# Kernel optimization log

Hardware: AMD Instinct MI355X
Metric: run time of the kernel (lower is better)

## Reference

```python
import jax, jax.numpy as jnp
import numpy as np

B, T, D = 2, 2048, 1024   # batch, seq, d_model
E, K, H = 8, 2, 704       # routed experts, topk, expert hidden
SH = 704 * 2              # shared-expert hidden = moe_hidden * num_shared_experts
EPS = 1e-20               # topk_norm_epsilon
STD = 0.02                # init_weight_std


def setup_inputs() -> dict:
    key = jax.random.key(0)
    ks = jax.random.split(key, 8)
    return {
        "x":   jax.random.normal(ks[0], (B, T, D), jnp.float32),
        "Wg":  jax.random.normal(ks[1], (E, D), jnp.float32) * STD,   # router experts_weights
        "W1":  jax.random.normal(ks[2], (E, D, H), jnp.float32) * STD,  # gate proj per expert
        "W3":  jax.random.normal(ks[3], (E, D, H), jnp.float32) * STD,  # up proj per expert
        "W2":  jax.random.normal(ks[4], (E, H, D), jnp.float32) * STD,  # down proj per expert
        "Ws1": jax.random.normal(ks[5], (D, SH), jnp.float32) * STD,    # shared expert
        "Ws3": jax.random.normal(ks[6], (D, SH), jnp.float32) * STD,
        "Ws2": jax.random.normal(ks[7], (SH, D), jnp.float32) * STD,
    }


def reference(x, Wg, W1, W3, W2, Ws1, Ws3, Ws2):
    b, t, d = x.shape
    n = b * t
    xf = x.reshape(n, d)
    # softmax gating + topk + scatter back into dense [N,E] gate matrix
    gates = jax.nn.softmax(xf @ Wg.T, axis=-1)                      # [N,E]
    top_v, top_i = jax.lax.top_k(gates, K)                          # [N,K]
    masked = jnp.zeros_like(gates).at[jnp.arange(n)[:, None], top_i].set(top_v)
    masked = masked / (masked.sum(-1, keepdims=True) + EPS)         # normalized_moe_gates
    # per-expert SwiGLU FFN over all tokens, then gate-weighted combine
    h = jnp.einsum('nd,edh->enh', xf, W1)                           # [E,N,H]
    g = jnp.einsum('nd,edh->enh', xf, W3)
    y = jnp.einsum('enh,ehd->end', jax.nn.silu(h) * g, W2)          # [E,N,D]
    routed = jnp.einsum('ne,end->nd', masked, y)                    # combine
    shared = (jax.nn.silu(xf @ Ws1) * (xf @ Ws3)) @ Ws2             # shared experts
    return (routed + shared).reshape(b, t, d)
```

## Files before the change

### kernel.cpp

```cpp
#include <hip/hip_runtime.h>
#include <math.h>

typedef __bf16 bf16;
typedef __attribute__((ext_vector_type(8))) __bf16 bf16x8;
typedef __attribute__((ext_vector_type(4))) __bf16 bf16x4;
typedef __attribute__((ext_vector_type(4))) float f32x4;

#define NTOK 4096
#define DM   1024
#define NE   8
#define NEX  10
#define HE   704

#define MAP1_CAP 224
#define MAP2_CAP 160

#define OFF_CNT   0u
#define OFF_TOK   256u
#define OFF_WGT   131328u
#define OFF_XB    262400u
#define OFF_W1T   8651008u
#define OFF_W3T   20185344u
#define OFF_W2T   31719680u
#define OFF_WS1T  43254016u
#define OFF_WS3T  46137600u
#define OFF_WS2T  49021184u
#define OFF_ACT   51904768u
#define OFF_EIDS  74973440u
#define OFF_MAP1  OFF_EIDS
#define OFF_MAP2  (OFF_EIDS + 8192u)
#define OFF_GW    74989824u
#define OFF_SLOT  75022592u
#define OFF_YR    OFF_W1T

__device__ __forceinline__ void async_cp16(const bf16* g, bf16* l)
{
    __builtin_amdgcn_global_load_lds(
        (const __attribute__((address_space(1))) unsigned int*)g,
        (__attribute__((address_space(3))) unsigned int*)l, 16, 0, 0);
}

__global__ __launch_bounds__(256) void prep_all(
    const float* __restrict__ x,  const float* __restrict__ Wg,
    const float* __restrict__ W1, const float* __restrict__ W3, const float* __restrict__ W2,
    const float* __restrict__ Ws1, const float* __restrict__ Ws3, const float* __restrict__ Ws2,
    bf16* __restrict__ w1t, bf16* __restrict__ w3t, bf16* __restrict__ w2t,
    bf16* __restrict__ ws1t, bf16* __restrict__ ws3t, bf16* __restrict__ ws2t,
    bf16* __restrict__ xb, int* __restrict__ eids, float2* __restrict__ gw)
{
    int id = blockIdx.x;
    if (id < 21120) {
        const float* src; bf16* dst; int C, rt, ct, nkt;
        if (id < 5632)       { int t = id;         int e = t / 704, m = t % 704; C = 704;
                               src = W1 + (size_t)e * 1024 * 704;  dst = w1t + (size_t)e * 720896;
                               ct = m % 22; rt = m / 22; nkt = 32; }
        else if (id < 11264) { int t = id - 5632;  int e = t / 704, m = t % 704; C = 704;
                               src = W3 + (size_t)e * 1024 * 704;  dst = w3t + (size_t)e * 720896;
                               ct = m % 22; rt = m / 22; nkt = 32; }
        else if (id < 16896) { int t = id - 11264; int e = t / 704, m = t % 704; C = 1024;
                               src = W2 + (size_t)e * 704 * 1024;  dst = w2t + (size_t)e * 720896;
                               ct = m % 32; rt = m / 32; nkt = 22; }
        else if (id < 18304) { int t = id - 16896; C = 1408; src = Ws1;
                               ct = t % 44; rt = t / 44; nkt = 32;
                               int ep = (ct >= 22) ? 1 : 0; ct -= 22 * ep;
                               src += (size_t)704 * ep;
                               dst = ws1t + (size_t)ep * 720896; }
        else if (id < 19712) { int t = id - 18304; C = 1408; src = Ws3;
                               ct = t % 44; rt = t / 44; nkt = 32;
                               int ep = (ct >= 22) ? 1 : 0; ct -= 22 * ep;
                               src += (size_t)704 * ep;
                               dst = ws3t + (size_t)ep * 720896; }
        else                 { int t = id - 19712; C = 1024; src = Ws2;
                               ct = t % 32; rt = t / 32; nkt = 22;
                               int ep = (rt >= 22) ? 1 : 0; rt -= 22 * ep;
                               src += (size_t)704 * 1024 * ep;
                               dst = ws2t + (size_t)ep * 720896; }

        __shared__ float tl[32][33];
        int c0 = ct * 32, r0 = rt * 32;
        int row  = threadIdx.x >> 3;
        int col4 = (threadIdx.x & 7) * 4;
        float4 v = *(const float4*)&src[(size_t)(r0 + row) * C + c0 + col4];
        tl[row][col4 + 0] = v.x; tl[row][col4 + 1] = v.y;
        tl[row][col4 + 2] = v.z; tl[row][col4 + 3] = v.w;
        __syncthreads();
        int t2   = threadIdx.x;
        int half = t2 >> 7;
        int ei   = (t2 & 127) * 4;
        int cc   = ei >> 7;
        int nr   = (ei >> 3) & 15;
        int jj   = ei & 7;
        int n_loc = half * 16 + nr;
        int k_loc = cc * 8 + jj;
        bf16x4 o;
        o[0] = (bf16)tl[k_loc + 0][n_loc];
        o[1] = (bf16)tl[k_loc + 1][n_loc];
        o[2] = (bf16)tl[k_loc + 2][n_loc];
        o[3] = (bf16)tl[k_loc + 3][n_loc];
        int ng = ct * 2 + half;
        *(bf16x4*)&dst[(size_t)(((ng * nkt + rt) << 9) + ei)] = o;
        return;
    }
    id -= 21120;
    if (id < 4096) {
        int i = id * 256 + threadIdx.x;
        float4 v = ((const float4*)x)[i];
        bf16x4 o;
        o[0] = (bf16)v.x; o[1] = (bf16)v.y; o[2] = (bf16)v.z; o[3] = (bf16)v.w;
        ((bf16x4*)xb)[i] = o;
        return;
    }
    id -= 4096;
    {
        int n    = id * 4 + (threadIdx.x >> 6);
        int lane = threadIdx.x & 63;
        const float* xrow = x + (size_t)n * DM;
        float xr[16];
        #pragma unroll
        for (int j = 0; j < 16; j++) xr[j] = xrow[lane + 64 * j];
        float logit[NE];
        #pragma unroll
        for (int e = 0; e < NE; e++) {
            const float* wr = Wg + e * DM;
            float s = 0.f;
            #pragma unroll
            for (int j = 0; j < 16; j++) s += xr[j] * wr[lane + 64 * j];
            #pragma unroll
            for (int off = 32; off; off >>= 1) s += __shfl_xor(s, off, 64);
            logit[e] = s;
        }
        if (lane == 0) {
            int i0 = 0;
            #pragma unroll
            for (int e = 1; e < NE; e++) if (logit[e] > logit[i0]) i0 = e;
            int i1 = (i0 == 0) ? 1 : 0;
            #pragma unroll
            for (int e = 0; e < NE; e++) if (e != i0 && logit[e] > logit[i1]) i1 = e;
            float m = logit[0];
            #pragma unroll
            for (int e = 1; e < NE; e++) m = fmaxf(m, logit[e]);
            float denom = 0.f;
            #pragma unroll
            for (int e = 0; e < NE; e++) denom += expf(logit[e] - m);
            float g0 = expf(logit[i0] - m) / denom;
            float g1 = expf(logit[i1] - m) / denom;
            float inv = 1.f / (g0 + g1 + 1e-20f);
            eids[n] = i0 | (i1 << 16);
            gw[n] = make_float2(g0 * inv, g1 * inv);
        }
    }
}

__global__ __launch_bounds__(128) void build_lists(
    const int* __restrict__ eids, const float2* __restrict__ gw,
    int* __restrict__ cnt, int* __restrict__ tok, float* __restrict__ wgt,
    int2* __restrict__ slots)
{
    __shared__ int lcnt[NE];
    __shared__ int gbase[NE];
    int t = threadIdx.x;
    int n = blockIdx.x * 128 + t;
    if (t < NE) lcnt[t] = 0;
    __syncthreads();
    int packed = eids[n];
    float2 w = gw[n];
    int e0 = packed & 0xffff, e1 = packed >> 16;
    int s0 = atomicAdd(&lcnt[e0], 1);
    int s1 = atomicAdd(&lcnt[e1], 1);
    __syncthreads();
    if (t < NE) gbase[t] = atomicAdd(&cnt[t], lcnt[t]);
    __syncthreads();
    int p0 = gbase[e0] + s0, p1 = gbase[e1] + s1;
    tok[e0 * NTOK + p0] = n; wgt[e0 * NTOK + p0] = w.x;
    tok[e1 * NTOK + p1] = n; wgt[e1 * NTOK + p1] = w.y;
    slots[n] = make_int2((e0 << 16) | p0, (e1 << 16) | p1);
}

__global__ void prefix_kernel(const int* __restrict__ cnt, int* __restrict__ pfx,
                              int* __restrict__ map1, int* __restrict__ map2)
{
    __shared__ int sx1[144], ss1[144], se1[144];
    __shared__ int sx2[112], ss2[112], se2[112];
    __shared__ int ns1s, ns2s;
    int t = threadIdx.x;
    for (int i = t; i < 8 * MAP1_CAP; i += 64) map1[i] = -1;
    for (int i = t; i < 8 * MAP2_CAP; i += 64) map2[i] = -1;

    if (t == 0) {
        int s = 0;
        for (int e = 0; e < NEX; e++) { pfx[e] = s; s += (e < NE) ? cnt[e] : NTOK; }
        pfx[NEX] = s;

        int ntl[NEX];
        int tot1 = 0;
        for (int e = 0; e < NEX; e++) {
            int c = (e < NE) ? cnt[e] : NTOK;
            ntl[e] = (c + 127) >> 7;
            tot1 += ntl[e];
        }
        {
            int len[8] = {0,0,0,0,0,0,0,0};
            int avg = (tot1 * 11 + 7) >> 3;
            int ns = 0, k = 0;
            for (int e = 0; e < NEX; e++) {
                k = 0;
                for (int q = 1; q < 8; q++) if (len[q] < len[k]) k = q;
                for (int tt = 0; tt < ntl[e]; tt++) {
                    if (len[k] >= avg) {
                        k = 0;
                        for (int q = 1; q < 8; q++) if (len[q] < len[k]) k = q;
                    }
                    if (len[k] + 11 > MAP1_CAP) {
                        k = 0;
                        for (int q = 1; q < 8; q++) if (len[q] < len[k]) k = q;
                    }
                    sx1[ns] = k; ss1[ns] = len[k]; se1[ns] = (e << 20) | (tt << 8);
                    len[k] += 11; ns++;
                }
            }
            ns1s = ns;
        }
        {
            int wrk[8] = {0,0,0,0,0,0,0,0};
            int slt[8] = {0,0,0,0,0,0,0,0};
            int totw = 0;
            for (int e = 0; e <= NE; e++)
                totw += (e < NE) ? ntl[e] * 8 * 22 : (NTOK >> 7) * 8 * 44;
            int avg = (totw + 7) >> 3;
            int ns = 0, k = 0;
            for (int e = 0; e <= NE; e++) {
                int nt2 = (e < NE) ? ntl[e] : (NTOK >> 7);
                int wpd = (e < NE) ? 22 : 44;
                k = 0;
                for (int q = 1; q < 8; q++) if (wrk[q] < wrk[k]) k = q;
                for (int tt = 0; tt < nt2; tt++) {
                    if (wrk[k] >= avg) {
                        k = 0;
                        for (int q = 1; q < 8; q++) if (wrk[q] < wrk[k]) k = q;
                    }
                    if (slt[k] + 8 > MAP2_CAP) {
                        k = 0;
                        for (int q = 1; q < 8; q++) if (slt[q] < slt[k]) k = q;
                    }
                    sx2[ns] = k; ss2[ns] = slt[k]; se2[ns] = (e << 20) | (tt << 8);
                    slt[k] += 8; wrk[k] += 8 * wpd; ns++;
                }
            }
            ns2s = ns;
        }
    }
    __syncthreads();
    int n1 = ns1s, n2 = ns2s;
    for (int i = t; i < n1 * 11; i += 64) {
        int sg = i / 11, h = i - sg * 11;
        map1[(ss1[sg] + h) * 8 + sx1[sg]] = se1[sg] | h;
    }
    for (int i = t; i < n2 * 8; i += 64) {
        int sg = i >> 3, d = i & 7;
        map2[(ss2[sg] + d) * 8 + sx2[sg]] = se2[sg] | d;
    }
}

__global__ __launch_bounds__(256) void gemm1_swiglu(
    const bf16* __restrict__ xb,
    const bf16* __restrict__ w1t, const bf16* __restrict__ w3t,
    const bf16* __restrict__ ws1t, const bf16* __restrict__ ws3t,
    bf16* __restrict__ act,
    const int* __restrict__ cnt, const int* __restrict__ pfx,
    const int* __restrict__ tok, const int* __restrict__ map)
{
    int b = blockIdx.x;
    int ent = map[(b >> 3) * 8 + (b & 7)];
    if (ent < 0) return;
    int e  = ent >> 20;
    int m0 = ((ent >> 8) & 0xfff) << 7;
    int h0 = (ent & 255) * 64;
    int count = (e < NE) ? cnt[e] : NTOK;
    int base = pfx[e];
    const bf16 *B1, *B3;
    if (e < NE) { B1 = w1t + (size_t)e * 720896;         B3 = w3t + (size_t)e * 720896; }
    else        { B1 = ws1t + (size_t)(e - NE) * 720896; B3 = ws3t + (size_t)(e - NE) * 720896; }
    const int* tlist = (e < NE) ? tok + e * NTOK : nullptr;

    __shared__ bf16 As[3][8 * 512];
    __shared__ bf16 B1s[3][4 * 512];
    __shared__ bf16 B3s[3][4 * 512];

    int tid = threadIdx.x, w = tid >> 6, lane = tid & 63;

    int r3 = lane >> 2;
    int cx = (lane & 3) ^ ((r3 >> 1) & 3);
    int sA0 = m0 + 32 * w + r3, sA1 = sA0 + 16;
    int rA0 = tlist ? (sA0 < count ? tlist[sA0] : 0) : (sA0 < count ? sA0 : 0);
    int rA1 = tlist ? (sA1 < count ? tlist[sA1] : 0) : (sA1 < count ? sA1 : 0);
    const bf16* ga0 = xb + (size_t)rA0 * DM + cx * 8;
    const bf16* ga1 = xb + (size_t)rA1 * DM + cx * 8;
    const bf16* gb1 = B1 + ((size_t)((h0 >> 4) + w) * 32) * 512 + lane * 8;
    const bf16* gb3 = B3 + ((size_t)((h0 >> 4) + w) * 32) * 512 + lane * 8;
    bf16* aA0 = &As[0][0]  + (2 * w) * 512;
    bf16* aA1 = aA0 + 512;
    bf16* aB1 = &B1s[0][0] + w * 512;
    bf16* aB3 = &B3s[0][0] + w * 512;

    int rl = lane & 15, ch = lane >> 4;
    int uA = 4 * rl + (ch ^ ((rl >> 1) & 3));
    int gA = (w & 1) * 4;
    int gB = (w >> 1) * 2;
    int wm = (w & 1) * 64, wn = (w >> 1) * 32;

    f32x4 acch[4][2], accg[4][2];
    #pragma unroll
    for (int i = 0; i < 4; i++)
        #pragma unroll
        for (int j = 0; j < 2; j++) {
            acch[i][j] = (f32x4){0.f, 0.f, 0.f, 0.f};
            accg[i][j] = (f32x4){0.f, 0.f, 0.f, 0.f};
        }

#define STAGE1(bs) do { \
        async_cp16(ga0, aA0 + (bs) * 4096); \
        async_cp16(ga1, aA1 + (bs) * 4096); \
        async_cp16(gb1, aB1 + (bs) * 2048); \
        async_cp16(gb3, aB3 + (bs) * 2048); \
        ga0 += 32; ga1 += 32; gb1 += 512; gb3 += 512; \
    } while (0)

    STAGE1(0);
    STAGE1(1);
    asm volatile("s_waitcnt vmcnt(4)" ::: "memory");
    __builtin_amdgcn_s_barrier();

    int rb = 0, sb = 2;
    for (int k0 = 0; k0 < 32; k0++) {
        const bf16* Ab  = &As[0][0]  + rb * 4096;
        const bf16* B1b = &B1s[0][0] + rb * 2048;
        const bf16* B3b = &B3s[0][0] + rb * 2048;
        bf16x8 af[4], b1f[2], b3f[2];
        #pragma unroll
        for (int i = 0; i < 4; i++) af[i] = *(const bf16x8*)(Ab + (gA + i) * 512 + uA * 8);
        #pragma unroll
        for (int j = 0; j < 2; j++) {
            b1f[j] = *(const bf16x8*)(B1b + (gB + j) * 512 + lane * 8);
            b3f[j] = *(const bf16x8*)(B3b + (gB + j) * 512 + lane * 8);
        }
        if (k0 < 30) STAGE1(sb);
        #pragma unroll
        for (int i = 0; i < 4; i++)
            #pragma unroll
            for (int j = 0; j < 2; j++) {
                acch[i][j] = __builtin_amdgcn_mfma_f32_16x16x32_bf16(af[i], b1f[j], acch[i][j], 0, 0, 0);
                accg[i][j] = __builtin_amdgcn_mfma_f32_16x16x32_bf16(af[i], b3f[j], accg[i][j], 0, 0, 0);
            }
        if (k0 < 30)       asm volatile("s_waitcnt vmcnt(4)" ::: "memory");
        else if (k0 == 30) asm volatile("s_waitcnt vmcnt(0)" ::: "memory");
        __builtin_amdgcn_sched_barrier(0);
        __builtin_amdgcn_s_barrier();
        rb = (rb == 2) ? 0 : rb + 1;
        sb = (sb == 2) ? 0 : sb + 1;
    }
#undef STAGE1

    #pragma unroll
    for (int i = 0; i < 4; i++)
        #pragma unroll
        for (int j = 0; j < 2; j++)
            #pragma unroll
            for (int r = 0; r < 4; r++) {
                int row = wm + i * 16 + ch * 4 + r;
                int s2 = m0 + row;
                if (s2 < count) {
                    float hv = acch[i][j][r], gv = accg[i][j][r];
                    float a = hv / (1.f + expf(-hv)) * gv;
                    act[(size_t)(base + s2) * HE + h0 + wn + j * 16 + rl] = (bf16)a;
                }
            }
}

__global__ __launch_bounds__(256) void gemm2_all(
    const bf16* __restrict__ act,
    const bf16* __restrict__ w2t, const bf16* __restrict__ ws2t,
    bf16* __restrict__ yr, float* __restrict__ out,
    const int* __restrict__ cnt, const int* __restrict__ pfx,
    const float* __restrict__ wgt, const int* __restrict__ map)
{
    int b = blockIdx.x;
    int ent = map[(b >> 3) * 8 + (b & 7)];
    if (ent < 0) return;
    int e  = ent >> 20;
    int m0 = ((ent >> 8) & 0xfff) << 7;
    int d0 = (ent & 255) * 128;

    __shared__ bf16 As[3][8 * 512];
    __shared__ bf16 Bs[3][8 * 512];

    int tid = threadIdx.x, w = tid >> 6, lane = tid & 63;

    int r3 = lane >> 2;
    int cx = (lane & 3) ^ ((r3 >> 1) & 3);
    int sA0 = m0 + 32 * w + r3, sA1 = sA0 + 16;
    int rl = lane & 15, ch = lane >> 4;
    int uA = 4 * rl + (ch ^ ((rl >> 1) & 3));
    int gA = (w & 1) * 4, gB = (w >> 1) * 4;
    int wm = (w & 1) * 64, wn = (w >> 1) * 64;

    bf16* aA0 = &As[0][0] + (2 * w) * 512;
    bf16* aA1 = aA0 + 512;
    bf16* aB0 = &Bs[0][0] + (2 * w) * 512;
    bf16* aB1 = aB0 + 512;

    int count, base; const bf16* Bp;
    if (e < NE) { count = cnt[e]; base = pfx[e]; Bp = w2t + (size_t)e * 720896; }
    else        { count = NTOK;   base = NTOK * 2; Bp = ws2t; }

    int a0 = (sA0 < count) ? (base + sA0) : base;
    int a1 = (sA1 < count) ? (base + sA1) : base;
    const bf16* ga0 = act + (size_t)a0 * HE + cx * 8;
    const bf16* ga1 = act + (size_t)a1 * HE + cx * 8;
    const bf16* gb0 = Bp + ((size_t)((d0 >> 4) + 2 * w) * 22) * 512 + lane * 8;
    const bf16* gb1 = Bp + ((size_t)((d0 >> 4) + 2 * w + 1) * 22) * 512 + lane * 8;

    f32x4 acc[4][4];
    #pragma unroll
    for (int i = 0; i < 4; i++)
        #pragma unroll
        for (int j = 0; j < 4; j++) acc[i][j] = (f32x4){0.f, 0.f, 0.f, 0.f};

#define STAGE2(bs) do { \
        async_cp16(ga0, aA0 + (bs) * 4096); \
        async_cp16(ga1, aA1 + (bs) * 4096); \
        async_cp16(gb0, aB0 + (bs) * 4096); \
        async_cp16(gb1, aB1 + (bs) * 4096); \
        ga0 += 32; ga1 += 32; gb0 += 512; gb1 += 512; \
    } while (0)

    int total = (e < NE) ? 22 : 44;
    STAGE2(0);
    STAGE2(1);
    asm volatile("s_waitcnt vmcnt(4)" ::: "memory");
    __builtin_amdgcn_s_barrier();

    int rb = 0, sb = 2;
    for (int kt = 0; kt < total; kt++) {
        const bf16* Ab = &As[0][0] + rb * 4096;
        const bf16* Bb = &Bs[0][0] + rb * 4096;
        bf16x8 af[4], bf_[4];
        #pragma unroll
        for (int i = 0; i < 4; i++) af[i]  = *(const bf16x8*)(Ab + (gA + i) * 512 + uA * 8);
        #pragma unroll
        for (int j = 0; j < 4; j++) bf_[j] = *(const bf16x8*)(Bb + (gB + j) * 512 + lane * 8);
        int nx = kt + 2;
        if (nx < total) {
            if (nx == 22) {
                ga0 = act + (size_t)(12288 + sA0) * HE + cx * 8;
                ga1 = act + (size_t)(12288 + sA1) * HE + cx * 8;
                const bf16* B2 = ws2t + 720896;
                gb0 = B2 + ((size_t)((d0 >> 4) + 2 * w) * 22) * 512 + lane * 8;
                gb1 = B2 + ((size_t)((d0 >> 4) + 2 * w + 1) * 22) * 512 + lane * 8;
            }
            STAGE2(sb);
        }
        #pragma unroll
        for (int i = 0; i < 4; i++)
            #pragma unroll
            for (int j = 0; j < 4; j++)
                acc[i][j] = __builtin_amdgcn_mfma_f32_16x16x32_bf16(af[i], bf_[j], acc[i][j], 0, 0, 0);
        if (nx < total)       asm volatile("s_waitcnt vmcnt(4)" ::: "memory");
        else if (nx == total) asm volatile("s_waitcnt vmcnt(0)" ::: "memory");
        __builtin_amdgcn_sched_barrier(0);
        __builtin_amdgcn_s_barrier();
        rb = (rb == 2) ? 0 : rb + 1;
        sb = (sb == 2) ? 0 : sb + 1;
    }
#undef STAGE2

    if (e < NE) {
        const float* wl = wgt + e * NTOK;
        #pragma unroll
        for (int i = 0; i < 4; i++) {
            #pragma unroll
            for (int r = 0; r < 4; r++) {
                int row = wm + i * 16 + ch * 4 + r;
                int s2 = m0 + row;
                if (s2 < count) {
                    float wt = wl[s2];
                    bf16* yrow = yr + (size_t)(base + s2) * DM + d0 + wn;
                    #pragma unroll
                    for (int j = 0; j < 4; j++)
                        yrow[j * 16 + rl] = (bf16)(wt * acc[i][j][r]);
                }
            }
        }
    } else {
        #pragma unroll
        for (int i = 0; i < 4; i++) {
            #pragma unroll
            for (int r = 0; r < 4; r++) {
                int row = wm + i * 16 + ch * 4 + r;
                float* orow = out + (size_t)(m0 + row) * DM + d0 + wn;
                #pragma unroll
                for (int j = 0; j < 4; j++)
                    orow[j * 16 + rl] = acc[i][j][r];
            }
        }
    }
}

__global__ __launch_bounds__(256) void fuse_add(
    const bf16* __restrict__ yr, const int2* __restrict__ slots,
    const int* __restrict__ pfx, float* __restrict__ out)
{
    int n = blockIdx.x;
    int2 s = slots[n];
    int slot0 = pfx[s.x >> 16] + (s.x & 0xffff);
    int slot1 = pfx[s.y >> 16] + (s.y & 0xffff);
    const bf16* y0 = yr + (size_t)slot0 * DM;
    const bf16* y1 = yr + (size_t)slot1 * DM;
    float* orow = out + (size_t)n * DM;
    int d = threadIdx.x * 4;
    bf16x4 a = *(const bf16x4*)(y0 + d);
    bf16x4 b = *(const bf16x4*)(y1 + d);
    float4 o = *(float4*)(orow + d);
    o.x += (float)a[0] + (float)b[0];
    o.y += (float)a[1] + (float)b[1];
    o.z += (float)a[2] + (float)b[2];
    o.w += (float)a[3] + (float)b[3];
    *(float4*)(orow + d) = o;
}

extern "C" void kernel_launch(void* const* d_in, const int* in_sizes, int n_in,
                              void* d_out, int out_size, void* d_ws, size_t ws_size,
                              hipStream_t stream)
{
    const float* x   = (const float*)d_in[0];
    const float* Wg  = (const float*)d_in[1];
    const float* W1  = (const float*)d_in[2];
    const float* W3  = (const float*)d_in[3];
    const float* W2  = (const float*)d_in[4];
    const float* Ws1 = (const float*)d_in[5];
    const float* Ws3 = (const float*)d_in[6];
    const float* Ws2 = (const float*)d_in[7];
    float* out = (float*)d_out;
    char*  ws  = (char*)d_ws;

    int*    cnt   = (int*)(ws + OFF_CNT);
    int*    pfx   = (int*)(ws + OFF_CNT + 32);
    int*    tok   = (int*)(ws + OFF_TOK);
    float*  wgt   = (float*)(ws + OFF_WGT);
    bf16*   xb    = (bf16*)(ws + OFF_XB);
    bf16*   w1t   = (bf16*)(ws + OFF_W1T);
    bf16*   w3t   = (bf16*)(ws + OFF_W3T);
    bf16*   w2t   = (bf16*)(ws + OFF_W2T);
    bf16*   ws1t  = (bf16*)(ws + OFF_WS1T);
    bf16*   ws3t  = (bf16*)(ws + OFF_WS3T);
    bf16*   ws2t  = (bf16*)(ws + OFF_WS2T);
    bf16*   act   = (bf16*)(ws + OFF_ACT);
    int*    eids  = (int*)(ws + OFF_EIDS);
    int*    map1  = (int*)(ws + OFF_MAP1);
    int*    map2  = (int*)(ws + OFF_MAP2);
    float2* gw    = (float2*)(ws + OFF_GW);
    int2*   slots = (int2*)(ws + OFF_SLOT);
    bf16*   yr    = (bf16*)(ws + OFF_YR);

    hipMemsetAsync(ws, 0, 256, stream);

    prep_all<<<21120 + 4096 + 1024, 256, 0, stream>>>(
        x, Wg, W1, W3, W2, Ws1, Ws3, Ws2,
        w1t, w3t, w2t, ws1t, ws3t, ws2t, xb, eids, gw);

    build_lists<<<32, 128, 0, stream>>>(eids, gw, cnt, tok, wgt, slots);
    prefix_kernel<<<1, 64, 0, stream>>>(cnt, pfx, map1, map2);

    gemm1_swiglu<<<8 * MAP1_CAP, 256, 0, stream>>>(
        xb, w1t, w3t, ws1t, ws3t, act, cnt, pfx, tok, map1);

    gemm2_all<<<8 * MAP2_CAP, 256, 0, stream>>>(
        act, w2t, ws2t, yr, out, cnt, pfx, wgt, map2);

    fuse_add<<<NTOK, 256, 0, stream>>>(yr, slots, pfx, out);
}
```

Measured before the change: 308.6 us.

## Fuse routing kernels into one block and deepen GEMM pipelines to four stages

Replaces the memset, the list-building kernel and the prefix kernel with a single 1024-thread block that counts, scatters and builds the schedule maps in one launch using shared-memory atomics only. Both grouped GEMM kernels move from triple to quadruple LDS buffering, with three stages prefetched and adjusted waitcnt thresholds. This removes two launches and hides more global-load latency. The cost is more LDS per block, which may reduce occupancy, and a serial single-block routing step.

After: 309.0 us. About the same (+0.1%).

```diff
diff --git a/kernel.cpp b/kernel.cpp
--- a/kernel.cpp
+++ b/kernel.cpp
@@ -151,50 +151,44 @@
     }
 }
 
-__global__ __launch_bounds__(128) void build_lists(
+__global__ __launch_bounds__(1024) void route_all(
     const int* __restrict__ eids, const float2* __restrict__ gw,
-    int* __restrict__ cnt, int* __restrict__ tok, float* __restrict__ wgt,
-    int2* __restrict__ slots)
+    int* __restrict__ cnt, int* __restrict__ pfx,
+    int* __restrict__ tok, float* __restrict__ wgt, int2* __restrict__ slots,
+    int* __restrict__ map1, int* __restrict__ map2)
 {
     __shared__ int lcnt[NE];
-    __shared__ int gbase[NE];
-    int t = threadIdx.x;
-    int n = blockIdx.x * 128 + t;
-    if (t < NE) lcnt[t] = 0;
-    __syncthreads();
-    int packed = eids[n];
-    float2 w = gw[n];
-    int e0 = packed & 0xffff, e1 = packed >> 16;
-    int s0 = atomicAdd(&lcnt[e0], 1);
-    int s1 = atomicAdd(&lcnt[e1], 1);
-    __syncthreads();
-    if (t < NE) gbase[t] = atomicAdd(&cnt[t], lcnt[t]);
-    __syncthreads();
-    int p0 = gbase[e0] + s0, p1 = gbase[e1] + s1;
-    tok[e0 * NTOK + p0] = n; wgt[e0 * NTOK + p0] = w.x;
-    tok[e1 * NTOK + p1] = n; wgt[e1 * NTOK + p1] = w.y;
-    slots[n] = make_int2((e0 << 16) | p0, (e1 << 16) | p1);
-}
-
-__global__ void prefix_kernel(const int* __restrict__ cnt, int* __restrict__ pfx,
-                              int* __restrict__ map1, int* __restrict__ map2)
-{
     __shared__ int sx1[144], ss1[144], se1[144];
     __shared__ int sx2[112], ss2[112], se2[112];
     __shared__ int ns1s, ns2s;
     int t = threadIdx.x;
-    for (int i = t; i < 8 * MAP1_CAP; i += 64) map1[i] = -1;
-    for (int i = t; i < 8 * MAP2_CAP; i += 64) map2[i] = -1;
-
+    if (t < NE) lcnt[t] = 0;
+    __syncthreads();
+    #pragma unroll
+    for (int c = 0; c < 4; c++) {
+        int n = c * 1024 + t;
+        int packed = eids[n];
+        float2 w = gw[n];
+        int e0 = packed & 0xffff, e1 = packed >> 16;
+        int p0 = atomicAdd(&lcnt[e0], 1);
+        int p1 = atomicAdd(&lcnt[e1], 1);
+        tok[e0 * NTOK + p0] = n; wgt[e0 * NTOK + p0] = w.x;
+        tok[e1 * NTOK + p1] = n; wgt[e1 * NTOK + p1] = w.y;
+        slots[n] = make_int2((e0 << 16) | p0, (e1 << 16) | p1);
+    }
+    __syncthreads();
+    if (t < NE) cnt[t] = lcnt[t];
+    for (int i = t; i < 8 * MAP1_CAP; i += 1024) map1[i] = -1;
+    for (int i = t; i < 8 * MAP2_CAP; i += 1024) map2[i] = -1;
     if (t == 0) {
         int s = 0;
-        for (int e = 0; e < NEX; e++) { pfx[e] = s; s += (e < NE) ? cnt[e] : NTOK; }
+        for (int e = 0; e < NEX; e++) { pfx[e] = s; s += (e < NE) ? lcnt[e] : NTOK; }
         pfx[NEX] = s;
 
         int ntl[NEX];
         int tot1 = 0;
         for (int e = 0; e < NEX; e++) {
-            int c = (e < NE) ? cnt[e] : NTOK;
+            int c = (e < NE) ? lcnt[e] : NTOK;
             ntl[e] = (c + 127) >> 7;
             tot1 += ntl[e];
         }
@@ -251,11 +245,11 @@
     }
     __syncthreads();
     int n1 = ns1s, n2 = ns2s;
-    for (int i = t; i < n1 * 11; i += 64) {
+    for (int i = t; i < n1 * 11; i += 1024) {
         int sg = i / 11, h = i - sg * 11;
         map1[(ss1[sg] + h) * 8 + sx1[sg]] = se1[sg] | h;
     }
-    for (int i = t; i < n2 * 8; i += 64) {
+    for (int i = t; i < n2 * 8; i += 1024) {
         int sg = i >> 3, d = i & 7;
         map2[(ss2[sg] + d) * 8 + sx2[sg]] = se2[sg] | d;
     }
@@ -282,9 +276,9 @@
     else        { B1 = ws1t + (size_t)(e - NE) * 720896; B3 = ws3t + (size_t)(e - NE) * 720896; }
     const int* tlist = (e < NE) ? tok + e * NTOK : nullptr;
 
-    __shared__ bf16 As[3][8 * 512];
-    __shared__ bf16 B1s[3][4 * 512];
-    __shared__ bf16 B3s[3][4 * 512];
+    __shared__ bf16 As[4][8 * 512];
+    __shared__ bf16 B1s[4][4 * 512];
+    __shared__ bf16 B3s[4][4 * 512];
 
     int tid = threadIdx.x, w = tid >> 6, lane = tid & 63;
 
@@ -325,12 +319,11 @@
         ga0 += 32; ga1 += 32; gb1 += 512; gb3 += 512; \
     } while (0)
 
-    STAGE1(0);
-    STAGE1(1);
-    asm volatile("s_waitcnt vmcnt(4)" ::: "memory");
+    STAGE1(0); STAGE1(1); STAGE1(2);
+    asm volatile("s_waitcnt vmcnt(8)" ::: "memory");
     __builtin_amdgcn_s_barrier();
 
-    int rb = 0, sb = 2;
+    int rb = 0, sb = 3;
     for (int k0 = 0; k0 < 32; k0++) {
         const bf16* Ab  = &As[0][0]  + rb * 4096;
         const bf16* B1b = &B1s[0][0] + rb * 2048;
@@ -343,7 +336,7 @@
             b1f[j] = *(const bf16x8*)(B1b + (gB + j) * 512 + lane * 8);
             b3f[j] = *(const bf16x8*)(B3b + (gB + j) * 512 + lane * 8);
         }
-        if (k0 < 30) STAGE1(sb);
+        if (k0 <= 28) STAGE1(sb);
         #pragma unroll
         for (int i = 0; i < 4; i++)
             #pragma unroll
@@ -351,12 +344,13 @@
                 acch[i][j] = __builtin_amdgcn_mfma_f32_16x16x32_bf16(af[i], b1f[j], acch[i][j], 0, 0, 0);
                 accg[i][j] = __builtin_amdgcn_mfma_f32_16x16x32_bf16(af[i], b3f[j], accg[i][j], 0, 0, 0);
             }
-        if (k0 < 30)       asm volatile("s_waitcnt vmcnt(4)" ::: "memory");
+        if (k0 <= 28)      asm volatile("s_waitcnt vmcnt(8)" ::: "memory");
+        else if (k0 == 29) asm volatile("s_waitcnt vmcnt(4)" ::: "memory");
         else if (k0 == 30) asm volatile("s_waitcnt vmcnt(0)" ::: "memory");
         __builtin_amdgcn_sched_barrier(0);
         __builtin_amdgcn_s_barrier();
-        rb = (rb == 2) ? 0 : rb + 1;
-        sb = (sb == 2) ? 0 : sb + 1;
+        rb = (rb + 1) & 3;
+        sb = (sb + 1) & 3;
     }
 #undef STAGE1
 
@@ -390,8 +384,8 @@
     int m0 = ((ent >> 8) & 0xfff) << 7;
     int d0 = (ent & 255) * 128;
 
-    __shared__ bf16 As[3][8 * 512];
-    __shared__ bf16 Bs[3][8 * 512];
+    __shared__ bf16 As[4][8 * 512];
+    __shared__ bf16 Bs[4][8 * 512];
 
     int tid = threadIdx.x, w = tid >> 6, lane = tid & 63;
 
@@ -434,12 +428,11 @@
     } while (0)
 
     int total = (e < NE) ? 22 : 44;
-    STAGE2(0);
-    STAGE2(1);
-    asm volatile("s_waitcnt vmcnt(4)" ::: "memory");
+    STAGE2(0); STAGE2(1); STAGE2(2);
+    asm volatile("s_waitcnt vmcnt(8)" ::: "memory");
     __builtin_amdgcn_s_barrier();
 
-    int rb = 0, sb = 2;
+    int rb = 0, sb = 3;
     for (int kt = 0; kt < total; kt++) {
         const bf16* Ab = &As[0][0] + rb * 4096;
         const bf16* Bb = &Bs[0][0] + rb * 4096;
@@ -448,7 +441,7 @@
         for (int i = 0; i < 4; i++) af[i]  = *(const bf16x8*)(Ab + (gA + i) * 512 + uA * 8);
         #pragma unroll
         for (int j = 0; j < 4; j++) bf_[j] = *(const bf16x8*)(Bb + (gB + j) * 512 + lane * 8);
-        int nx = kt + 2;
+        int nx = kt + 3;
         if (nx < total) {
             if (nx == 22) {
                 ga0 = act + (size_t)(12288 + sA0) * HE + cx * 8;
@@ -464,12 +457,13 @@
             #pragma unroll
             for (int j = 0; j < 4; j++)
                 acc[i][j] = __builtin_amdgcn_mfma_f32_16x16x32_bf16(af[i], bf_[j], acc[i][j], 0, 0, 0);
-        if (nx < total)       asm volatile("s_waitcnt vmcnt(4)" ::: "memory");
-        else if (nx == total) asm volatile("s_waitcnt vmcnt(0)" ::: "memory");
+        if (kt <= total - 4)      asm volatile("s_waitcnt vmcnt(8)" ::: "memory");
+        else if (kt == total - 3) asm volatile("s_waitcnt vmcnt(4)" ::: "memory");
+        else if (kt == total - 2) asm volatile("s_waitcnt vmcnt(0)" ::: "memory");
         __builtin_amdgcn_sched_barrier(0);
         __builtin_amdgcn_s_barrier();
-        rb = (rb == 2) ? 0 : rb + 1;
-        sb = (sb == 2) ? 0 : sb + 1;
+        rb = (rb + 1) & 3;
+        sb = (sb + 1) & 3;
     }
 #undef STAGE2
 
@@ -561,14 +555,11 @@
     int2*   slots = (int2*)(ws + OFF_SLOT);
     bf16*   yr    = (bf16*)(ws + OFF_YR);
 
-    hipMemsetAsync(ws, 0, 256, stream);
-
     prep_all<<<21120 + 4096 + 1024, 256, 0, stream>>>(
         x, Wg, W1, W3, W2, Ws1, Ws3, Ws2,
         w1t, w3t, w2t, ws1t, ws3t, ws2t, xb, eids, gw);
 
-    build_lists<<<32, 128, 0, stream>>>(eids, gw, cnt, tok, wgt, slots);
-    prefix_kernel<<<1, 64, 0, stream>>>(cnt, pfx, map1, map2);
+    route_all<<<1, 1024, 0, stream>>>(eids, gw, cnt, pfx, tok, wgt, slots, map1, map2);
 
     gemm1_swiglu<<<8 * MAP1_CAP, 256, 0, stream>>>(
         xb, w1t, w3t, ws1t, ws3t, act, cnt, pfx, tok, map1);
```
